# Optimization experiments

Hardware: AMD Instinct MI355X
Metric: run time of the kernel (lower is better)

Reference implementation:

```python
import jax, jax.numpy as jnp
import numpy as np


def setup_inputs() -> dict:
    key = jax.random.key(0)
    k1, k2, k3 = jax.random.split(key, 3)
    n_sup, n_qry, d, n_classes = 512, 2097152, 64, 16
    support_features = jax.random.normal(k1, (n_sup, d), dtype=jnp.float32)
    query_features = jax.random.normal(k2, (n_qry, d), dtype=jnp.float32)
    support_labels = jnp.arange(n_sup, dtype=jnp.int64) % n_classes  # every class populated
    query_labels = jax.random.randint(k3, (n_qry,), 0, n_classes, dtype=jnp.int64)
    return {
        "support_features": support_features,
        "query_features": query_features,
        "support_labels": support_labels,
        "query_labels": query_labels,
        "n_classes": n_classes,
        "n_iter": 50,
        "beta": 5,
    }


def _sq_dists(q, q_sq, centroids):
    # squared Euclidean distances [Nq, C]; q_sq precomputed row norms of q
    return q_sq[:, None] - 2.0 * (q @ centroids.T) + jnp.sum(centroids * centroids, axis=-1)[None, :]


def reference(support_features, query_features, support_labels, query_labels, n_classes, n_iter, beta):
    dtype = support_features.dtype
    beta_f = jnp.asarray(beta, dtype)
    # per-class support sums/counts (hard assignments, fixed across iterations)
    oh = jax.nn.one_hot(support_labels, n_classes, dtype=dtype)        # [Ns, C]
    class_counts = jnp.sum(oh, axis=0)                                  # [C]
    sup_sum = oh.T @ support_features                                   # [C, d]
    centroids = sup_sum / class_counts[:, None]                         # class means init

    q_sq = jnp.sum(query_features * query_features, axis=-1)            # [Nq]

    def step(centroids, _):
        d2 = _sq_dists(query_features, q_sq, centroids)                 # [Nq, C]
        w = jax.nn.softmax(-beta_f * d2, axis=-1)                       # soft assignments
        num = sup_sum + w.T @ query_features                            # [C, d]
        den = class_counts + jnp.sum(w, axis=0)                         # [C]
        return num / den[:, None], None

    centroids, _ = jax.lax.scan(step, centroids, None, length=n_iter)

    d2 = _sq_dists(query_features, q_sq, centroids)
    pred = jnp.argmin(d2, axis=-1)
    acc = jnp.mean((pred == query_labels).astype(jnp.float32))
    return acc
```

## Files before the change

### kernel.cpp

```cpp
#include <hip/hip_runtime.h>
#include <stdint.h>

typedef short bf16x8 __attribute__((ext_vector_type(8)));
typedef float f32x4 __attribute__((ext_vector_type(4)));
typedef uint32_t u32x4 __attribute__((ext_vector_type(4)));
typedef unsigned short u16;

#define ITERS 50
#define BETA_F 5.0f

#define WS_SUPSUM 0
#define WS_COUNTS 1024
#define WS_CENT   1040
#define WS_CSQ    2064
#define WS_ACC    2080
#define WS_CORR   10400
#define WS_QB_OFF 10432

__device__ __forceinline__ u16 f2bf(float x) {
  union { float f; uint32_t u; } v; v.f = x;
  uint32_t r = (v.u + 0x7FFFu + ((v.u >> 16) & 1u)) >> 16;
  return (u16)r;
}
__device__ __forceinline__ float bf2f(u16 b) {
  union { float f; uint32_t u; } v; v.u = ((uint32_t)b) << 16;
  return v.f;
}
__device__ __forceinline__ uint32_t fkey(float f) {
  union { float f; uint32_t u; } v; v.f = f;
  return (v.u & 0x80000000u) ? ~v.u : (v.u | 0x80000000u);
}

template <int CTRL>
__device__ __forceinline__ float dppf(float x) {
  int i = __builtin_bit_cast(int, x);
  int r = __builtin_amdgcn_update_dpp(i, i, CTRL, 0xF, 0xF, false);
  return __builtin_bit_cast(float, r);
}
template <int CTRL>
__device__ __forceinline__ uint32_t dppu(uint32_t x) {
  int r = __builtin_amdgcn_update_dpp((int)x, (int)x, CTRL, 0xF, 0xF, false);
  return (uint32_t)r;
}
__device__ __forceinline__ float rmax16(float x) {
  x = fmaxf(x, dppf<0xB1>(x));
  x = fmaxf(x, dppf<0x4E>(x));
  x = fmaxf(x, dppf<0x141>(x));
  x = fmaxf(x, dppf<0x140>(x));
  return x;
}
__device__ __forceinline__ float rsum16(float x) {
  x += dppf<0xB1>(x);
  x += dppf<0x4E>(x);
  x += dppf<0x141>(x);
  x += dppf<0x140>(x);
  return x;
}
__device__ __forceinline__ uint32_t rumax16(uint32_t x) {
  uint32_t t;
  t = dppu<0xB1>(x);  x = (t > x) ? t : x;
  t = dppu<0x4E>(x);  x = (t > x) ? t : x;
  t = dppu<0x141>(x); x = (t > x) ? t : x;
  t = dppu<0x140>(x); x = (t > x) ? t : x;
  return x;
}

__global__ __launch_bounds__(1024) void init_kernel(const float* __restrict__ sup,
                                                    const int* __restrict__ slab,
                                                    int NS, float* __restrict__ ws) {
  const int tid = threadIdx.x;
  const int c = tid >> 6, j = tid & 63;
  float s = 0.f; int cnt = 0;
  for (int i = 0; i < NS; ++i) {
    int lbl = slab[i];
    float v = sup[i * 64 + j];
    if (lbl == c) { s += v; cnt++; }
  }
  ws[WS_SUPSUM + tid] = s;
  if (j == 0) ws[WS_COUNTS + c] = (float)cnt;
  ws[WS_CENT + tid] = s / (float)cnt;
  for (int i = tid; i < 8 * 1040; i += 1024) ws[WS_ACC + i] = 0.f;
  if (tid == 0) ws[WS_CORR] = 0.f;
  __syncthreads();
  if (j == 0) {
    float sq = 0.f;
    for (int k = 0; k < 64; ++k) { float v = ws[WS_CENT + c * 64 + k]; sq += v * v; }
    ws[WS_CSQ + c] = sq;
  }
}

__global__ __launch_bounds__(256) void convert_kernel(const float* __restrict__ qf,
                                                      u16* __restrict__ qb, int n) {
  const int start = blockIdx.x * 256 + threadIdx.x;
  const int stride = gridDim.x * 256;
  const float4* in = (const float4*)qf;
  uint2* out = (uint2*)qb;
  for (int k = start; k < (n >> 2); k += stride) {
    float4 v = in[k];
    uint32_t p0 = (uint32_t)f2bf(v.x) | ((uint32_t)f2bf(v.y) << 16);
    uint32_t p1 = (uint32_t)f2bf(v.z) | ((uint32_t)f2bf(v.w) << 16);
    out[k] = make_uint2(p0, p1);
  }
}

template <bool SRC_BF16>
__global__ __launch_bounds__(256, 4) void pass_kernel(const float* __restrict__ qf,
                                                      const u16* __restrict__ qb,
                                                      int NQ, float* __restrict__ ws) {
  __shared__ __attribute__((aligned(16))) uint32_t qt_w[4][64][16];
  __shared__ __attribute__((aligned(16))) u16 w_lds[4][16][32];
  __shared__ float redden[16];

  const int tid = threadIdx.x;
  const int lane = tid & 63;
  const int wv = tid >> 6;
  const int c = lane & 15;
  const int g = lane >> 4;

  const float* cent = ws + WS_CENT;
  bf16x8 bc0, bc1;
#pragma unroll
  for (int j = 0; j < 8; ++j) {
    bc0[j] = (short)f2bf(cent[c * 64 + g * 8 + j]);
    bc1[j] = (short)f2bf(cent[c * 64 + 32 + g * 8 + j]);
  }
  const float csq = ws[WS_CSQ + c];

  f32x4 acc[4];
#pragma unroll
  for (int nt = 0; nt < 4; ++nt) acc[nt] = (f32x4){0.f, 0.f, 0.f, 0.f};
  float denacc = 0.f;

  const uint32_t psel = (c & 1) ? 0x03020706u : 0x05040100u;

  const int wave_id = blockIdx.x * 4 + wv;
  const int nwaves = gridDim.x * 4;
  const int ntiles = NQ >> 5;

  for (int tile = wave_id; tile < ntiles; tile += nwaves) {
    const int qbase = tile << 5;
#pragma unroll
    for (int st = 0; st < 2; ++st) {
      const int q = qbase + st * 16 + c;
      bf16x8 a0, a1;
      if (SRC_BF16) {
        const u16* qrow = qb + (size_t)q * 64;
        a0 = *(const bf16x8*)(qrow + g * 8);
        a1 = *(const bf16x8*)(qrow + 32 + g * 8);
      } else {
        const float* qrow = qf + (size_t)q * 64;
#pragma unroll
        for (int j = 0; j < 8; ++j) {
          a0[j] = (short)f2bf(qrow[g * 8 + j]);
          a1[j] = (short)f2bf(qrow[32 + g * 8 + j]);
        }
      }
      f32x4 sc = (f32x4){0.f, 0.f, 0.f, 0.f};
      sc = __builtin_amdgcn_mfma_f32_16x16x32_bf16(a0, bc0, sc, 0, 0, 0);
      sc = __builtin_amdgcn_mfma_f32_16x16x32_bf16(a1, bc1, sc, 0, 0, 0);
      u16 wq[4];
#pragma unroll
      for (int r = 0; r < 4; ++r) {
        float sv = BETA_F * (2.f * sc[r] - csq);
        float m = rmax16(sv);
        float e = __expf(sv - m);
        float sum = rsum16(e);
        float w = e * __builtin_amdgcn_rcpf(sum);
        wq[r] = f2bf(w);
        denacc += bf2f(wq[r]);
      }
      {
        uint32_t lo = (uint32_t)wq[0] | ((uint32_t)wq[1] << 16);
        uint32_t hi = (uint32_t)wq[2] | ((uint32_t)wq[3] << 16);
        *(uint2*)&w_lds[wv][c][st * 16 + g * 4] = make_uint2(lo, hi);
      }
      const int drow = g * 8 + (c & 1);
      const int wcol = ((st << 3) + (c >> 1)) ^ (g << 2);
      u32x4 ua = __builtin_bit_cast(u32x4, a0);
      u32x4 ub = __builtin_bit_cast(u32x4, a1);
#pragma unroll
      for (int p = 0; p < 4; ++p) {
        uint32_t m0 = ua[p];
        uint32_t n0 = (uint32_t)__builtin_amdgcn_update_dpp((int)m0, (int)m0, 0xB1, 0xF, 0xF, false);
        qt_w[wv][drow + 2 * p][wcol] = __builtin_amdgcn_perm(n0, m0, psel);
        uint32_t m1 = ub[p];
        uint32_t n1 = (uint32_t)__builtin_amdgcn_update_dpp((int)m1, (int)m1, 0xB1, 0xF, 0xF, false);
        qt_w[wv][32 + drow + 2 * p][wcol] = __builtin_amdgcn_perm(n1, m1, psel);
      }
    }
    bf16x8 aw = *(const bf16x8*)&w_lds[wv][c][g * 8];
#pragma unroll
    for (int nt = 0; nt < 4; ++nt) {
      const int K = ((nt << 1) + (c >> 3)) & 3;
      bf16x8 bq = *(const bf16x8*)&qt_w[wv][nt * 16 + c][(g ^ K) << 2];
      acc[nt] = __builtin_amdgcn_mfma_f32_16x16x32_bf16(aw, bq, acc[nt], 0, 0, 0);
    }
  }

  __syncthreads();
  float* red = (float*)&qt_w[0][0][0];
  for (int i = tid; i < 1024; i += 256) red[i] = 0.f;
  if (tid < 16) redden[tid] = 0.f;
  __syncthreads();
#pragma unroll
  for (int nt = 0; nt < 4; ++nt)
#pragma unroll
    for (int r = 0; r < 4; ++r)
      atomicAdd(&red[(g * 4 + r) * 64 + nt * 16 + c], acc[nt][r]);
  atomicAdd(&redden[c], denacc);
  __syncthreads();
  float* accn = ws + WS_ACC + (size_t)(blockIdx.x & 7) * 1040;
  for (int i = tid; i < 1024; i += 256) atomicAdd(&accn[i], red[i]);
  if (tid < 16) atomicAdd(&accn[1024 + tid], redden[tid]);
}

__global__ __launch_bounds__(1024) void update_kernel(float* __restrict__ ws) {
  const int tid = threadIdx.x;
  const int c = tid >> 6;
  float num = ws[WS_SUPSUM + tid];
  float den = ws[WS_COUNTS + c];
#pragma unroll
  for (int rep = 0; rep < 8; ++rep) {
    num += ws[WS_ACC + rep * 1040 + tid];
    den += ws[WS_ACC + rep * 1040 + 1024 + c];
  }
  ws[WS_CENT + tid] = num / den;
  for (int i = tid; i < 8 * 1040; i += 1024) ws[WS_ACC + i] = 0.f;
  __syncthreads();
  if ((tid & 63) == 0) {
    float sq = 0.f;
    for (int k = 0; k < 64; ++k) { float v = ws[WS_CENT + c * 64 + k]; sq += v * v; }
    ws[WS_CSQ + c] = sq;
  }
}

template <bool SRC_BF16>
__global__ __launch_bounds__(256, 4) void final_kernel(const float* __restrict__ qf,
                                                       const u16* __restrict__ qb,
                                                       const int* __restrict__ qlab,
                                                       int NQ, float* __restrict__ ws) {
  const int tid = threadIdx.x;
  const int lane = tid & 63;
  const int c = lane & 15;
  const int g = lane >> 4;

  const float* cent = ws + WS_CENT;
  bf16x8 bc0, bc1;
#pragma unroll
  for (int j = 0; j < 8; ++j) {
    bc0[j] = (short)f2bf(cent[c * 64 + g * 8 + j]);
    bc1[j] = (short)f2bf(cent[c * 64 + 32 + g * 8 + j]);
  }
  const float csq = ws[WS_CSQ + c];

  int cnt = 0;
  const int wave_id = blockIdx.x * 4 + (tid >> 6);
  const int nwaves = gridDim.x * 4;
  const int ntiles = NQ >> 4;

  for (int tile = wave_id; tile < ntiles; tile += nwaves) {
    const int qbase = tile << 4;
    const int q = qbase + c;
    bf16x8 a0, a1;
    if (SRC_BF16) {
      const u16* qrow = qb + (size_t)q * 64;
      a0 = *(const bf16x8*)(qrow + g * 8);
      a1 = *(const bf16x8*)(qrow + 32 + g * 8);
    } else {
      const float* qrow = qf + (size_t)q * 64;
#pragma unroll
      for (int j = 0; j < 8; ++j) {
        a0[j] = (short)f2bf(qrow[g * 8 + j]);
        a1[j] = (short)f2bf(qrow[32 + g * 8 + j]);
      }
    }
    f32x4 sc = (f32x4){0.f, 0.f, 0.f, 0.f};
    sc = __builtin_amdgcn_mfma_f32_16x16x32_bf16(a0, bc0, sc, 0, 0, 0);
    sc = __builtin_amdgcn_mfma_f32_16x16x32_bf16(a1, bc1, sc, 0, 0, 0);
#pragma unroll
    for (int r = 0; r < 4; ++r) {
      float val = 2.f * sc[r] - csq;
      uint32_t key = (fkey(val) & 0xFFFFFFF0u) | (uint32_t)(15 - c);
      key = rumax16(key);
      int pred = 15 - (int)(key & 15u);
      if (c == 0) cnt += (qlab[qbase + g * 4 + r] == pred) ? 1 : 0;
    }
  }
#pragma unroll
  for (int msk = 1; msk < 64; msk <<= 1) cnt += __shfl_xor(cnt, msk);
  if (lane == 0) atomicAdd(&ws[WS_CORR], (float)cnt);
}

__global__ void finalize_kernel(const float* __restrict__ ws, float* __restrict__ out, float inv) {
  out[0] = ws[WS_CORR] * inv;
}

extern "C" void kernel_launch(void* const* d_in, const int* in_sizes, int n_in,
                              void* d_out, int out_size, void* d_ws, size_t ws_size,
                              hipStream_t stream) {
  const float* sup = (const float*)d_in[0];
  const float* qf  = (const float*)d_in[1];
  const int* slab  = (const int*)d_in[2];
  const int* qlab  = (const int*)d_in[3];
  float* ws = (float*)d_ws;
  float* out = (float*)d_out;
  const int NS = in_sizes[0] / 64;
  const int NQ = in_sizes[1] / 64;
  u16* qb = (u16*)(ws + WS_QB_OFF);
  const size_t need = (size_t)WS_QB_OFF * 4 + (size_t)NQ * 64 * 2;
  const bool use_bf = (ws_size >= need);

  init_kernel<<<1, 1024, 0, stream>>>(sup, slab, NS, ws);
  if (use_bf) convert_kernel<<<4096, 256, 0, stream>>>(qf, qb, NQ * 64);
  for (int it = 0; it < ITERS; ++it) {
    if (use_bf) pass_kernel<true><<<2048, 256, 0, stream>>>(qf, qb, NQ, ws);
    else        pass_kernel<false><<<2048, 256, 0, stream>>>(qf, qb, NQ, ws);
    update_kernel<<<1, 1024, 0, stream>>>(ws);
  }
  if (use_bf) final_kernel<true><<<2048, 256, 0, stream>>>(qf, qb, qlab, NQ, ws);
  else        final_kernel<false><<<2048, 256, 0, stream>>>(qf, qb, qlab, NQ, ws);
  finalize_kernel<<<1, 1, 0, stream>>>(ws, out, 1.0f / (float)NQ);
}
```

Measured before the change: 5.797 ms.

## Store queries as fp8 and split centroids into hi/lo fp8 for MFMA

Converts query features once to fp8 (halving per-iteration streaming bytes versus bf16) and computes query-centroid dot products with fp8 MFMAs, splitting each centroid into a hi and lo fp8 part to keep precision. The centroid squared norm is recomputed from the quantized values in-kernel, and fp8 queries are widened to bf16 for the weighted-sum MFMA. The final argmin pass reads fp32 queries directly. This trades extra MFMA and convert instructions, plus fp8 quantization error on queries, for less memory traffic across the 50 iterations.

Result: no change. 5.881 ms (+1.4%).

```diff
diff --git a/kernel.cpp b/kernel.cpp
--- a/kernel.cpp
+++ b/kernel.cpp
@@ -3,8 +3,11 @@
 
 typedef short bf16x8 __attribute__((ext_vector_type(8)));
 typedef float f32x4 __attribute__((ext_vector_type(4)));
+typedef float f32x2 __attribute__((ext_vector_type(2)));
 typedef uint32_t u32x4 __attribute__((ext_vector_type(4)));
+typedef uint32_t u32x2 __attribute__((ext_vector_type(2)));
 typedef unsigned short u16;
+typedef long long i64;
 
 #define ITERS 50
 #define BETA_F 5.0f
@@ -15,7 +18,7 @@
 #define WS_CSQ    2064
 #define WS_ACC    2080
 #define WS_CORR   10400
-#define WS_QB_OFF 10432
+#define WS_Q8_OFF 10432
 
 __device__ __forceinline__ u16 f2bf(float x) {
   union { float f; uint32_t u; } v; v.f = x;
@@ -26,9 +29,41 @@
   union { float f; uint32_t u; } v; v.u = ((uint32_t)b) << 16;
   return v.f;
 }
+__device__ __forceinline__ float u2f(uint32_t u) {
+  union { float f; uint32_t u; } v; v.u = u;
+  return v.f;
+}
 __device__ __forceinline__ uint32_t fkey(float f) {
   union { float f; uint32_t u; } v; v.f = f;
   return (v.u & 0x80000000u) ? ~v.u : (v.u | 0x80000000u);
+}
+__device__ __forceinline__ uint32_t cvt_pk_bf16(float a, float b) {
+  uint32_t r;
+  asm("v_cvt_pk_bf16_f32 %0, %1, %2" : "=v"(r) : "v"(a), "v"(b));
+  return r;
+}
+__device__ __forceinline__ uint32_t pk8(float a, float b, float c, float d) {
+  int r = __builtin_amdgcn_cvt_pk_fp8_f32(a, b, 0, false);
+  r = __builtin_amdgcn_cvt_pk_fp8_f32(c, d, r, true);
+  return (uint32_t)r;
+}
+__device__ __forceinline__ i64 pack64(uint32_t lo, uint32_t hi) {
+  return (i64)(((uint64_t)hi << 32) | (uint64_t)lo);
+}
+__device__ __forceinline__ void quant_hilo4(float v0, float v1, float v2, float v3,
+                                            uint32_t& hi, uint32_t& lo, float& sq) {
+  uint32_t h = pk8(v0, v1, v2, v3);
+  float h0 = __builtin_amdgcn_cvt_f32_fp8((int)h, 0);
+  float h1 = __builtin_amdgcn_cvt_f32_fp8((int)h, 1);
+  float h2 = __builtin_amdgcn_cvt_f32_fp8((int)h, 2);
+  float h3 = __builtin_amdgcn_cvt_f32_fp8((int)h, 3);
+  uint32_t l = pk8(v0 - h0, v1 - h1, v2 - h2, v3 - h3);
+  float c0 = h0 + __builtin_amdgcn_cvt_f32_fp8((int)l, 0);
+  float c1 = h1 + __builtin_amdgcn_cvt_f32_fp8((int)l, 1);
+  float c2 = h2 + __builtin_amdgcn_cvt_f32_fp8((int)l, 2);
+  float c3 = h3 + __builtin_amdgcn_cvt_f32_fp8((int)l, 3);
+  sq += c0 * c0 + c1 * c1 + c2 * c2 + c3 * c3;
+  hi = h; lo = l;
 }
 
 template <int CTRL>
@@ -90,22 +125,24 @@
 }
 
 __global__ __launch_bounds__(256) void convert_kernel(const float* __restrict__ qf,
-                                                      u16* __restrict__ qb, int n) {
+                                                      u32x4* __restrict__ q8, int n16) {
   const int start = blockIdx.x * 256 + threadIdx.x;
   const int stride = gridDim.x * 256;
-  const float4* in = (const float4*)qf;
-  uint2* out = (uint2*)qb;
-  for (int k = start; k < (n >> 2); k += stride) {
-    float4 v = in[k];
-    uint32_t p0 = (uint32_t)f2bf(v.x) | ((uint32_t)f2bf(v.y) << 16);
-    uint32_t p1 = (uint32_t)f2bf(v.z) | ((uint32_t)f2bf(v.w) << 16);
-    out[k] = make_uint2(p0, p1);
-  }
-}
-
-template <bool SRC_BF16>
+  const f32x4* in = (const f32x4*)qf;
+  for (int k = start; k < n16; k += stride) {
+    f32x4 v0 = in[4 * k + 0], v1 = in[4 * k + 1], v2 = in[4 * k + 2], v3 = in[4 * k + 3];
+    u32x4 o;
+    o[0] = pk8(v0[0], v0[1], v0[2], v0[3]);
+    o[1] = pk8(v1[0], v1[1], v1[2], v1[3]);
+    o[2] = pk8(v2[0], v2[1], v2[2], v2[3]);
+    o[3] = pk8(v3[0], v3[1], v3[2], v3[3]);
+    q8[k] = o;
+  }
+}
+
+template <bool SRC_F8>
 __global__ __launch_bounds__(256, 4) void pass_kernel(const float* __restrict__ qf,
-                                                      const u16* __restrict__ qb,
+                                                      const uint8_t* __restrict__ q8,
                                                       int NQ, float* __restrict__ ws) {
   __shared__ __attribute__((aligned(16))) uint32_t qt_w[4][64][16];
   __shared__ __attribute__((aligned(16))) u16 w_lds[4][16][32];
@@ -118,13 +155,17 @@
   const int g = lane >> 4;
 
   const float* cent = ws + WS_CENT;
-  bf16x8 bc0, bc1;
-#pragma unroll
-  for (int j = 0; j < 8; ++j) {
-    bc0[j] = (short)f2bf(cent[c * 64 + g * 8 + j]);
-    bc1[j] = (short)f2bf(cent[c * 64 + 32 + g * 8 + j]);
-  }
-  const float csq = ws[WS_CSQ + c];
+  const int cb = c * 64 + g * 8;
+  uint32_t bh0a, bl0a, bh0b, bl0b, bh1a, bl1a, bh1b, bl1b;
+  float csq = 0.f;
+  quant_hilo4(cent[cb + 0], cent[cb + 1], cent[cb + 2], cent[cb + 3], bh0a, bl0a, csq);
+  quant_hilo4(cent[cb + 4], cent[cb + 5], cent[cb + 6], cent[cb + 7], bh0b, bl0b, csq);
+  quant_hilo4(cent[cb + 32], cent[cb + 33], cent[cb + 34], cent[cb + 35], bh1a, bl1a, csq);
+  quant_hilo4(cent[cb + 36], cent[cb + 37], cent[cb + 38], cent[cb + 39], bh1b, bl1b, csq);
+  csq += __shfl_xor(csq, 16);
+  csq += __shfl_xor(csq, 32);
+  const i64 bh0 = pack64(bh0a, bh0b), bl0 = pack64(bl0a, bl0b);
+  const i64 bh1 = pack64(bh1a, bh1b), bl1 = pack64(bl1a, bl1b);
 
   f32x4 acc[4];
 #pragma unroll
@@ -142,49 +183,68 @@
 #pragma unroll
     for (int st = 0; st < 2; ++st) {
       const int q = qbase + st * 16 + c;
-      bf16x8 a0, a1;
-      if (SRC_BF16) {
-        const u16* qrow = qb + (size_t)q * 64;
-        a0 = *(const bf16x8*)(qrow + g * 8);
-        a1 = *(const bf16x8*)(qrow + 32 + g * 8);
+      u32x2 a0u, a1u;
+      if (SRC_F8) {
+        const uint8_t* qrow = q8 + (size_t)q * 64;
+        a0u = *(const u32x2*)(qrow + g * 8);
+        a1u = *(const u32x2*)(qrow + 32 + g * 8);
       } else {
-        const float* qrow = qf + (size_t)q * 64;
-#pragma unroll
-        for (int j = 0; j < 8; ++j) {
-          a0[j] = (short)f2bf(qrow[g * 8 + j]);
-          a1[j] = (short)f2bf(qrow[32 + g * 8 + j]);
-        }
+        const float* qrow = qf + (size_t)q * 64 + g * 8;
+        a0u[0] = pk8(qrow[0], qrow[1], qrow[2], qrow[3]);
+        a0u[1] = pk8(qrow[4], qrow[5], qrow[6], qrow[7]);
+        a1u[0] = pk8(qrow[32], qrow[33], qrow[34], qrow[35]);
+        a1u[1] = pk8(qrow[36], qrow[37], qrow[38], qrow[39]);
       }
+      const i64 a0 = __builtin_bit_cast(i64, a0u);
+      const i64 a1 = __builtin_bit_cast(i64, a1u);
       f32x4 sc = (f32x4){0.f, 0.f, 0.f, 0.f};
-      sc = __builtin_amdgcn_mfma_f32_16x16x32_bf16(a0, bc0, sc, 0, 0, 0);
-      sc = __builtin_amdgcn_mfma_f32_16x16x32_bf16(a1, bc1, sc, 0, 0, 0);
-      u16 wq[4];
+      sc = __builtin_amdgcn_mfma_f32_16x16x32_fp8_fp8(a0, bh0, sc, 0, 0, 0);
+      sc = __builtin_amdgcn_mfma_f32_16x16x32_fp8_fp8(a0, bl0, sc, 0, 0, 0);
+      sc = __builtin_amdgcn_mfma_f32_16x16x32_fp8_fp8(a1, bh1, sc, 0, 0, 0);
+      sc = __builtin_amdgcn_mfma_f32_16x16x32_fp8_fp8(a1, bl1, sc, 0, 0, 0);
+      float wr[4];
 #pragma unroll
       for (int r = 0; r < 4; ++r) {
         float sv = BETA_F * (2.f * sc[r] - csq);
         float m = rmax16(sv);
         float e = __expf(sv - m);
-        float sum = rsum16(e);
-        float w = e * __builtin_amdgcn_rcpf(sum);
-        wq[r] = f2bf(w);
-        denacc += bf2f(wq[r]);
+        float s = rsum16(e);
+        wr[r] = e * __builtin_amdgcn_rcpf(s);
       }
+      uint32_t wlo = cvt_pk_bf16(wr[0], wr[1]);
+      uint32_t whi = cvt_pk_bf16(wr[2], wr[3]);
+      *(uint2*)&w_lds[wv][c][st * 16 + g * 4] = make_uint2(wlo, whi);
+      denacc += u2f(wlo << 16) + u2f(wlo & 0xFFFF0000u) +
+                u2f(whi << 16) + u2f(whi & 0xFFFF0000u);
+
+      uint32_t ua[4], ub[4];
       {
-        uint32_t lo = (uint32_t)wq[0] | ((uint32_t)wq[1] << 16);
-        uint32_t hi = (uint32_t)wq[2] | ((uint32_t)wq[3] << 16);
-        *(uint2*)&w_lds[wv][c][st * 16 + g * 4] = make_uint2(lo, hi);
+        f32x2 t0 = __builtin_amdgcn_cvt_pk_f32_fp8((int)a0u[0], false);
+        f32x2 t1 = __builtin_amdgcn_cvt_pk_f32_fp8((int)a0u[0], true);
+        f32x2 t2 = __builtin_amdgcn_cvt_pk_f32_fp8((int)a0u[1], false);
+        f32x2 t3 = __builtin_amdgcn_cvt_pk_f32_fp8((int)a0u[1], true);
+        ua[0] = cvt_pk_bf16(t0[0], t0[1]);
+        ua[1] = cvt_pk_bf16(t1[0], t1[1]);
+        ua[2] = cvt_pk_bf16(t2[0], t2[1]);
+        ua[3] = cvt_pk_bf16(t3[0], t3[1]);
+        t0 = __builtin_amdgcn_cvt_pk_f32_fp8((int)a1u[0], false);
+        t1 = __builtin_amdgcn_cvt_pk_f32_fp8((int)a1u[0], true);
+        t2 = __builtin_amdgcn_cvt_pk_f32_fp8((int)a1u[1], false);
+        t3 = __builtin_amdgcn_cvt_pk_f32_fp8((int)a1u[1], true);
+        ub[0] = cvt_pk_bf16(t0[0], t0[1]);
+        ub[1] = cvt_pk_bf16(t1[0], t1[1]);
+        ub[2] = cvt_pk_bf16(t2[0], t2[1]);
+        ub[3] = cvt_pk_bf16(t3[0], t3[1]);
       }
       const int drow = g * 8 + (c & 1);
       const int wcol = ((st << 3) + (c >> 1)) ^ (g << 2);
-      u32x4 ua = __builtin_bit_cast(u32x4, a0);
-      u32x4 ub = __builtin_bit_cast(u32x4, a1);
 #pragma unroll
       for (int p = 0; p < 4; ++p) {
         uint32_t m0 = ua[p];
-        uint32_t n0 = (uint32_t)__builtin_amdgcn_update_dpp((int)m0, (int)m0, 0xB1, 0xF, 0xF, false);
+        uint32_t n0 = dppu<0xB1>(m0);
         qt_w[wv][drow + 2 * p][wcol] = __builtin_amdgcn_perm(n0, m0, psel);
         uint32_t m1 = ub[p];
-        uint32_t n1 = (uint32_t)__builtin_amdgcn_update_dpp((int)m1, (int)m1, 0xB1, 0xF, 0xF, false);
+        uint32_t n1 = dppu<0xB1>(m1);
         qt_w[wv][32 + drow + 2 * p][wcol] = __builtin_amdgcn_perm(n1, m1, psel);
       }
     }
@@ -234,9 +294,7 @@
   }
 }
 
-template <bool SRC_BF16>
 __global__ __launch_bounds__(256, 4) void final_kernel(const float* __restrict__ qf,
-                                                       const u16* __restrict__ qb,
                                                        const int* __restrict__ qlab,
                                                        int NQ, float* __restrict__ ws) {
   const int tid = threadIdx.x;
@@ -261,18 +319,12 @@
   for (int tile = wave_id; tile < ntiles; tile += nwaves) {
     const int qbase = tile << 4;
     const int q = qbase + c;
+    const float* qrow = qf + (size_t)q * 64;
     bf16x8 a0, a1;
-    if (SRC_BF16) {
-      const u16* qrow = qb + (size_t)q * 64;
-      a0 = *(const bf16x8*)(qrow + g * 8);
-      a1 = *(const bf16x8*)(qrow + 32 + g * 8);
-    } else {
-      const float* qrow = qf + (size_t)q * 64;
-#pragma unroll
-      for (int j = 0; j < 8; ++j) {
-        a0[j] = (short)f2bf(qrow[g * 8 + j]);
-        a1[j] = (short)f2bf(qrow[32 + g * 8 + j]);
-      }
+#pragma unroll
+    for (int j = 0; j < 8; ++j) {
+      a0[j] = (short)f2bf(qrow[g * 8 + j]);
+      a1[j] = (short)f2bf(qrow[32 + g * 8 + j]);
     }
     f32x4 sc = (f32x4){0.f, 0.f, 0.f, 0.f};
     sc = __builtin_amdgcn_mfma_f32_16x16x32_bf16(a0, bc0, sc, 0, 0, 0);
@@ -306,18 +358,17 @@
   float* out = (float*)d_out;
   const int NS = in_sizes[0] / 64;
   const int NQ = in_sizes[1] / 64;
-  u16* qb = (u16*)(ws + WS_QB_OFF);
-  const size_t need = (size_t)WS_QB_OFF * 4 + (size_t)NQ * 64 * 2;
-  const bool use_bf = (ws_size >= need);
+  uint8_t* q8 = (uint8_t*)(ws + WS_Q8_OFF);
+  const size_t need = (size_t)WS_Q8_OFF * 4 + (size_t)NQ * 64;
+  const bool use_f8 = (ws_size >= need);
 
   init_kernel<<<1, 1024, 0, stream>>>(sup, slab, NS, ws);
-  if (use_bf) convert_kernel<<<4096, 256, 0, stream>>>(qf, qb, NQ * 64);
+  if (use_f8) convert_kernel<<<4096, 256, 0, stream>>>(qf, (u32x4*)q8, NQ * 4);
   for (int it = 0; it < ITERS; ++it) {
-    if (use_bf) pass_kernel<true><<<2048, 256, 0, stream>>>(qf, qb, NQ, ws);
-    else        pass_kernel<false><<<2048, 256, 0, stream>>>(qf, qb, NQ, ws);
+    if (use_f8) pass_kernel<true><<<2048, 256, 0, stream>>>(qf, q8, NQ, ws);
+    else        pass_kernel<false><<<2048, 256, 0, stream>>>(qf, q8, NQ, ws);
     update_kernel<<<1, 1024, 0, stream>>>(ws);
   }
-  if (use_bf) final_kernel<true><<<2048, 256, 0, stream>>>(qf, qb, qlab, NQ, ws);
-  else        final_kernel<false><<<2048, 256, 0, stream>>>(qf, qb, qlab, NQ, ws);
+  final_kernel<<<2048, 256, 0, stream>>>(qf, qlab, NQ, ws);
   finalize_kernel<<<1, 1, 0, stream>>>(ws, out, 1.0f / (float)NQ);
 }
```
